# Kernel optimization log

Hardware: AMD Instinct MI355X
Metric: run time of the kernel (lower is better)

The kernel has to match this reference:

```python
import jax, jax.numpy as jnp
import numpy as np

# Module config (matches init_kwargs); num_heads must be 1 for the original
# torch code to type-check (score_proj: Linear(d_model, num_heads) applied to
# a head_dim-sized last axis, then squeeze(-1)).
B, S, D, H = 4, 512, 256, 1
DH = D // H  # head_dim == d_model when H == 1


def _linear_init(k, out_f, in_f):
    bound = 1.0 / np.sqrt(in_f)
    kw, kb = jax.random.split(k)
    W = jax.random.uniform(kw, (out_f, in_f), jnp.float32, -bound, bound)
    b = jax.random.uniform(kb, (out_f,), jnp.float32, -bound, bound)
    return W, b


def setup_inputs() -> dict:
    key = jax.random.key(0)
    ks = jax.random.split(key, 8)
    Wq, bq = _linear_init(ks[3], D, D)
    Wk, bk = _linear_init(ks[4], D, D)
    Wv, bv = _linear_init(ks[5], D, D)
    Ws, bs = _linear_init(ks[6], H, D)   # score_proj: d_model -> num_heads
    Wo, bo = _linear_init(ks[7], D, D)
    return {
        "query": jax.random.normal(ks[0], (B, S, D), jnp.float32),
        "key": jax.random.normal(ks[1], (B, S, D), jnp.float32),
        "value": jax.random.normal(ks[2], (B, S, D), jnp.float32),
        "Wq": Wq, "bq": bq, "Wk": Wk, "bk": bk, "Wv": Wv, "bv": bv,
        "Ws": Ws, "bs": bs, "Wo": Wo, "bo": bo,
    }


def reference(query, key, value, Wq, bq, Wk, bk, Wv, bv, Ws, bs, Wo, bo):
    b, s, _ = query.shape
    # Projections, split into heads: (B, H, S, DH)
    q = (query @ Wq.T + bq).reshape(b, s, H, DH).transpose(0, 2, 1, 3)
    k = (key @ Wk.T + bk).reshape(b, s, H, DH).transpose(0, 2, 1, 3)
    v = (value @ Wv.T + bv).reshape(b, s, H, DH).transpose(0, 2, 1, 3)
    # Bahdanau additive scores: tanh of pairwise sum -> (B, H, Sq, Sk, DH)
    t = jnp.tanh(q[:, :, :, None, :] + k[:, :, None, :, :])
    # score_proj (out_features == 1 when H == 1), then squeeze(-1)
    scores = jnp.einsum('bhqkd,od->bhqko', t, Ws) + bs  # (B,H,Sq,Sk,1)
    scores = scores[..., 0]                              # (B,H,Sq,Sk)
    attn = jax.nn.softmax(scores, axis=-1)
    # Weighted sum of values, merge heads back: (B, S, D)
    attended = jnp.einsum('bhqk,bhkd->bqhd', attn, v).reshape(b, s, D)
    out = attended @ Wo.T + bo  # dropout p=0.0 (eval) -> identity
    return out, attn
```

## Files before the change

### kernel.cpp

```cpp
#include <hip/hip_runtime.h>

typedef __attribute__((ext_vector_type(8))) short short8;
typedef __attribute__((ext_vector_type(4))) float f32x4;

constexpr int BATCH = 4;
constexpr int SEQ   = 512;
constexpr int DM    = 256;

#define MFMA(a,b,c) __builtin_amdgcn_mfma_f32_16x16x32_bf16((a),(b),(c),0,0,0)

__device__ __forceinline__ unsigned short bf16h(float x) {
    unsigned u = __float_as_uint(x);
    return (unsigned short)((u + 0x7FFF + ((u >> 16) & 1)) >> 16);
}
__device__ __forceinline__ float bf16f(unsigned short h) {
    return __uint_as_float(((unsigned)h) << 16);
}
__device__ __forceinline__ float exp2x_clamped(float x) {
    x = fminf(5.0f, fmaxf(-5.0f, x));
    return __builtin_amdgcn_exp2f(x * 2.8853900817779268f);
}
__device__ __forceinline__ void cvt8(const float* s, int4& h, int4& l) {
    unsigned hw[8], lw[8];
    #pragma unroll
    for (int j = 0; j < 8; ++j) {
        unsigned short hb = bf16h(s[j]);
        hw[j] = hb;
        lw[j] = bf16h(s[j] - bf16f(hb));
    }
    h.x = (int)(hw[0] | (hw[1] << 16)); h.y = (int)(hw[2] | (hw[3] << 16));
    h.z = (int)(hw[4] | (hw[5] << 16)); h.w = (int)(hw[6] | (hw[7] << 16));
    l.x = (int)(lw[0] | (lw[1] << 16)); l.y = (int)(lw[2] | (lw[3] << 16));
    l.z = (int)(lw[4] | (lw[5] << 16)); l.w = (int)(lw[6] | (lw[7] << 16));
}

template<int EPI, int ASRC, int BSRC>
__device__ __forceinline__ void mfma_core(
    const ushort* __restrict__ Ah, const ushort* __restrict__ Al,
    const float*  __restrict__ A0, const float*  __restrict__ A1, long ldA,
    const ushort* __restrict__ Bh, const ushort* __restrict__ Bl,
    const float*  __restrict__ B0, long ldB,
    float* __restrict__ C, long ldC, const float* __restrict__ bias,
    ushort* __restrict__ Th, ushort* __restrict__ Tl, long ldT)
{
    __shared__ short lds[32768];
    const int tid = threadIdx.x;
    const int i0 = tid, i1 = tid + 256;
    const int r0 = ((i0 >> 7) << 4) | (i0 & 15), r1 = ((i1 >> 7) << 4) | (i1 & 15);
    const int c0 = ((i0 >> 4) & 7) * 8,          c1 = ((i1 >> 4) & 7) * 8;
    const long a0o = (long)r0 * ldA + c0, a1o = (long)r1 * ldA + c1;
    const long b0o = (long)r0 * ldB + c0, b1o = (long)r1 * ldB + c1;

    int4 rah0, rah1, ral0, ral1, rbh0, rbh1, rbl0, rbl1;
    float4 fa00, fa01, fa10, fa11, ga00, ga01, ga10, ga11;
    float4 gb00, gb01, gb10, gb11;

    auto issue_loads = [&](int it) {
        long off = (long)it * 64;
        if constexpr (ASRC != 0) {
            fa00 = *(const float4*)(A0 + a0o + off); fa01 = *(const float4*)(A0 + a0o + off + 4);
            fa10 = *(const float4*)(A0 + a1o + off); fa11 = *(const float4*)(A0 + a1o + off + 4);
            if constexpr (ASRC == 2) {
                ga00 = *(const float4*)(A1 + a0o + off); ga01 = *(const float4*)(A1 + a0o + off + 4);
                ga10 = *(const float4*)(A1 + a1o + off); ga11 = *(const float4*)(A1 + a1o + off + 4);
            }
        } else {
            rah0 = *(const int4*)(Ah + a0o + off); rah1 = *(const int4*)(Ah + a1o + off);
            ral0 = *(const int4*)(Al + a0o + off); ral1 = *(const int4*)(Al + a1o + off);
        }
        if constexpr (BSRC == 1) {
            gb00 = *(const float4*)(B0 + b0o + off); gb01 = *(const float4*)(B0 + b0o + off + 4);
            gb10 = *(const float4*)(B0 + b1o + off); gb11 = *(const float4*)(B0 + b1o + off + 4);
        } else {
            rbh0 = *(const int4*)(Bh + b0o + off); rbh1 = *(const int4*)(Bh + b1o + off);
            rbl0 = *(const int4*)(Bl + b0o + off); rbl1 = *(const int4*)(Bl + b1o + off);
        }
    };
    auto write_lds = [&](int buf) {
        const int bo = buf * 16384;
        if constexpr (ASRC != 0) {
            float s0[8], s1[8];
            if constexpr (ASRC == 2) {
                s0[0]=fa00.x+ga00.x; s0[1]=fa00.y+ga00.y; s0[2]=fa00.z+ga00.z; s0[3]=fa00.w+ga00.w;
                s0[4]=fa01.x+ga01.x; s0[5]=fa01.y+ga01.y; s0[6]=fa01.z+ga01.z; s0[7]=fa01.w+ga01.w;
                s1[0]=fa10.x+ga10.x; s1[1]=fa10.y+ga10.y; s1[2]=fa10.z+ga10.z; s1[3]=fa10.w+ga10.w;
                s1[4]=fa11.x+ga11.x; s1[5]=fa11.y+ga11.y; s1[6]=fa11.z+ga11.z; s1[7]=fa11.w+ga11.w;
            } else {
                s0[0]=fa00.x; s0[1]=fa00.y; s0[2]=fa00.z; s0[3]=fa00.w;
                s0[4]=fa01.x; s0[5]=fa01.y; s0[6]=fa01.z; s0[7]=fa01.w;
                s1[0]=fa10.x; s1[1]=fa10.y; s1[2]=fa10.z; s1[3]=fa10.w;
                s1[4]=fa11.x; s1[5]=fa11.y; s1[6]=fa11.z; s1[7]=fa11.w;
            }
            int4 h, l2;
            cvt8(s0, h, l2);
            *(int4*)&lds[bo + i0 * 8] = h; *(int4*)&lds[bo + 4096 + i0 * 8] = l2;
            cvt8(s1, h, l2);
            *(int4*)&lds[bo + i1 * 8] = h; *(int4*)&lds[bo + 4096 + i1 * 8] = l2;
        } else {
            *(int4*)&lds[bo + i0 * 8] = rah0;        *(int4*)&lds[bo + i1 * 8] = rah1;
            *(int4*)&lds[bo + 4096 + i0 * 8] = ral0; *(int4*)&lds[bo + 4096 + i1 * 8] = ral1;
        }
        if constexpr (BSRC == 1) {
            float s0[8] = {gb00.x, gb00.y, gb00.z, gb00.w, gb01.x, gb01.y, gb01.z, gb01.w};
            float s1[8] = {gb10.x, gb10.y, gb10.z, gb10.w, gb11.x, gb11.y, gb11.z, gb11.w};
            int4 h, l2;
            cvt8(s0, h, l2);
            *(int4*)&lds[bo + 8192 + i0 * 8] = h; *(int4*)&lds[bo + 12288 + i0 * 8] = l2;
            cvt8(s1, h, l2);
            *(int4*)&lds[bo + 8192 + i1 * 8] = h; *(int4*)&lds[bo + 12288 + i1 * 8] = l2;
        } else {
            *(int4*)&lds[bo + 8192  + i0 * 8] = rbh0; *(int4*)&lds[bo + 8192  + i1 * 8] = rbh1;
            *(int4*)&lds[bo + 12288 + i0 * 8] = rbl0; *(int4*)&lds[bo + 12288 + i1 * 8] = rbl1;
        }
    };

    const int l = tid & 63, w = tid >> 6;
    const int ms = (w >> 1) * 2, ns = (w & 1) * 2;
    f32x4 acc00 = {0,0,0,0}, acc01 = {0,0,0,0}, acc10 = {0,0,0,0}, acc11 = {0,0,0,0};

    issue_loads(0);
    write_lds(0);
    __syncthreads();
    for (int it = 0; it < 4; ++it) {
        if (it < 3) issue_loads(it + 1);
        const int bo = (it & 1) * 16384;
        const int lo = l * 8;
        #pragma unroll
        for (int ks = 0; ks < 2; ++ks) {
            short8 a0h = *(const short8*)&lds[bo + ((ms    ) * 2 + ks) * 512 + lo];
            short8 a1h = *(const short8*)&lds[bo + ((ms + 1) * 2 + ks) * 512 + lo];
            short8 a0l = *(const short8*)&lds[bo + 4096 + ((ms    ) * 2 + ks) * 512 + lo];
            short8 a1l = *(const short8*)&lds[bo + 4096 + ((ms + 1) * 2 + ks) * 512 + lo];
            short8 b0h = *(const short8*)&lds[bo + 8192 + ((ns    ) * 2 + ks) * 512 + lo];
            short8 b1h = *(const short8*)&lds[bo + 8192 + ((ns + 1) * 2 + ks) * 512 + lo];
            short8 b0l = *(const short8*)&lds[bo + 12288 + ((ns    ) * 2 + ks) * 512 + lo];
            short8 b1l = *(const short8*)&lds[bo + 12288 + ((ns + 1) * 2 + ks) * 512 + lo];
            acc00 = MFMA(a0h, b0h, acc00); acc00 = MFMA(a0h, b0l, acc00); acc00 = MFMA(a0l, b0h, acc00);
            acc01 = MFMA(a0h, b1h, acc01); acc01 = MFMA(a0h, b1l, acc01); acc01 = MFMA(a0l, b1h, acc01);
            acc10 = MFMA(a1h, b0h, acc10); acc10 = MFMA(a1h, b0l, acc10); acc10 = MFMA(a1l, b0h, acc10);
            acc11 = MFMA(a1h, b1h, acc11); acc11 = MFMA(a1h, b1l, acc11); acc11 = MFMA(a1l, b1h, acc11);
        }
        if (it < 3) {
            write_lds((it + 1) & 1);
            __syncthreads();
        }
    }

    auto epi = [&](int i, int j, f32x4 a) {
        const int n  = (ns + j) * 16 + (l & 15);
        const int mb = (ms + i) * 16 + (l >> 4) * 4;
        if constexpr (EPI == 1) {
            float bb = bias[n];
            float x0 = a.x + bb, x1 = a.y + bb, x2 = a.z + bb, x3 = a.w + bb;
            unsigned short h0 = bf16h(x0), h1 = bf16h(x1), h2 = bf16h(x2), h3 = bf16h(x3);
            int2 ph, pl;
            ph.x = (int)(h0 | ((unsigned)h1 << 16));
            ph.y = (int)(h2 | ((unsigned)h3 << 16));
            pl.x = (int)(bf16h(x0 - bf16f(h0)) | ((unsigned)bf16h(x1 - bf16f(h1)) << 16));
            pl.y = (int)(bf16h(x2 - bf16f(h2)) | ((unsigned)bf16h(x3 - bf16f(h3)) << 16));
            *(int2*)&Th[(long)n * ldT + mb] = ph;
            *(int2*)&Tl[(long)n * ldT + mb] = pl;
        } else {
            float bb = (EPI == 2) ? 0.f : bias[n];
            float xs[4] = {a.x, a.y, a.z, a.w};
            #pragma unroll
            for (int r = 0; r < 4; ++r) {
                float x = xs[r] + bb;
                if constexpr (EPI == 0) x = exp2x_clamped(x);
                C[(long)(mb + r) * ldC + n] = x;
            }
        }
    };
    epi(0, 0, acc00); epi(0, 1, acc01); epi(1, 0, acc10); epi(1, 1, acc11);
}

__global__ __launch_bounds__(256) void proj_mfma(
    const float* __restrict__ q, const float* __restrict__ k, const float* __restrict__ v,
    const float* __restrict__ Wq, const float* __restrict__ Wk, const float* __restrict__ Wv,
    const float* bq, const float* bk, const float* bv,
    float* Eq, float* Ek, ushort* vpTh, ushort* vpTl)
{
    const int z = blockIdx.z;
    const long m0 = blockIdx.x * 64, n0 = blockIdx.y * 64;
    const float* A; const float* B; const float* bias;
    if (z == 0)      { A = q; B = Wq; bias = bq; }
    else if (z == 1) { A = k; B = Wk; bias = bk; }
    else             { A = v; B = Wv; bias = bv; }
    A += m0 * 256; B += n0 * 256; bias += n0;
    if (z < 2) {
        float* C = (z ? Ek : Eq) + m0 * 256 + n0;
        mfma_core<0, 1, 1>(nullptr, nullptr, A, nullptr, 256,
                           nullptr, nullptr, B, 256,
                           C, 256, bias, nullptr, nullptr, 0);
    } else {
        mfma_core<1, 1, 1>(nullptr, nullptr, A, nullptr, 256,
                           nullptr, nullptr, B, 256,
                           nullptr, 0, bias,
                           vpTh + n0 * 2048 + m0, vpTl + n0 * 2048 + m0, 2048);
    }
}

__global__ __launch_bounds__(256) void attnv_mfma(
    const ushort* attn_h, const ushort* attn_l,
    const ushort* vpTh, const ushort* vpTl, float* att0, float* att1)
{
    const int z = blockIdx.z, b = z >> 1, h = z & 1;
    const long m0 = blockIdx.x * 64, n0 = blockIdx.y * 64;
    const long arow = (long)b * SEQ + m0;
    const ushort* Ah = attn_h + arow * SEQ + h * 256;
    const ushort* Al = attn_l + arow * SEQ + h * 256;
    const ushort* Bh = vpTh + n0 * 2048 + (long)b * SEQ + h * 256;
    const ushort* Bl = vpTl + n0 * 2048 + (long)b * SEQ + h * 256;
    float* C = (h ? att1 : att0) + arow * DM + n0;
    mfma_core<2, 0, 0>(Ah, Al, nullptr, nullptr, SEQ,
                       Bh, Bl, nullptr, 2048,
                       C, DM, nullptr, nullptr, nullptr, 0);
}

__global__ __launch_bounds__(256) void out_mfma(
    const float* att0, const float* att1,
    const float* Wo, const float* bo, float* out)
{
    const long m0 = blockIdx.x * 64, n0 = blockIdx.y * 64;
    mfma_core<3, 2, 1>(nullptr, nullptr, att0 + m0 * 256, att1 + m0 * 256, 256,
                       nullptr, nullptr, Wo + n0 * 256, 256,
                       out + m0 * 256 + n0, 256, bo + n0, nullptr, nullptr, 0);
}

__global__ __launch_bounds__(256) void scores_kernel(
    const float* __restrict__ Eq, const float* __restrict__ Ek,
    const float* __restrict__ Ws, float* __restrict__ part)
{
    __shared__ __align__(16) float qL[64][68];
    __shared__ __align__(16) float kL[64][68];
    const int z = blockIdx.z;
    const int b = z >> 1, c = z & 1;
    const int q0 = blockIdx.x * 64, k0 = blockIdx.y * 64;
    const int tid = threadIdx.x;
    const int qi = tid >> 4, ki = tid & 15;

    float acc[4][4] = {};
    for (int cc = 0; cc < 2; ++cc) {
        const int c0 = c * 128 + cc * 64;
        const float* Eqb = Eq + ((long)b * SEQ + q0) * DM + c0;
        const float* Ekb = Ek + ((long)b * SEQ + k0) * DM + c0;
        if (cc) __syncthreads();
        #pragma unroll
        for (int i = 0; i < 4; ++i) {
            int f = i * 256 + tid;
            int r = f >> 4, col = (f & 15) << 2;
            *(float4*)&qL[r][col] = *(const float4*)(Eqb + (long)r * DM + col);
            *(float4*)&kL[r][col] = *(const float4*)(Ekb + (long)r * DM + col);
        }
        __syncthreads();
        #pragma unroll 2
        for (int d = 0; d < 64; d += 4) {
            float4 w4 = *(const float4*)(Ws + c0 + d);
            float4 av[4], bv[4];
            #pragma unroll
            for (int i = 0; i < 4; ++i) av[i] = *(const float4*)&qL[qi + 16 * i][d];
            #pragma unroll
            for (int j = 0; j < 4; ++j) bv[j] = *(const float4*)&kL[ki + 16 * j][d];
            #pragma unroll
            for (int i = 0; i < 4; ++i)
                #pragma unroll
                for (int j = 0; j < 4; ++j) {
                    float xp = fmaf(av[i].x, bv[j].x, 1.0f);
                    float yp = fmaf(av[i].y, bv[j].y, 1.0f);
                    float zp = fmaf(av[i].z, bv[j].z, 1.0f);
                    float wp = fmaf(av[i].w, bv[j].w, 1.0f);
                    float xy = xp * yp, zw = zp * wp;
                    float n1 = fmaf(w4.x, yp, w4.y * xp);
                    float n2 = fmaf(w4.z, wp, w4.w * zp);
                    float num = fmaf(n1, zw, n2 * xy);
                    acc[i][j] = fmaf(num, __builtin_amdgcn_rcpf(xy * zw), acc[i][j]);
                }
        }
    }

    float* pb = part + (long)c * (BATCH * SEQ * SEQ) + (long)b * SEQ * SEQ;
    #pragma unroll
    for (int i = 0; i < 4; ++i) {
        float* row = pb + (long)(q0 + qi + 16 * i) * SEQ + k0 + ki;
        #pragma unroll
        for (int j = 0; j < 4; ++j) row[16 * j] = acc[i][j];
    }
}

__global__ __launch_bounds__(256) void softmax_kernel(
    const float* __restrict__ part, float* __restrict__ attn,
    ushort* __restrict__ attn_h, ushort* __restrict__ attn_l)
{
    __shared__ float red[8];
    const int tid = threadIdx.x;
    const long row = blockIdx.x;
    constexpr long PS = (long)BATCH * SEQ * SEQ;
    const float* p = part + row * SEQ + tid * 2;
    float2 v0 = *(const float2*)(p);
    float2 v1 = *(const float2*)(p + PS);
    float sx = -2.0f * (v0.x + v1.x);
    float sy = -2.0f * (v0.y + v1.y);

    float m = fmaxf(sx, sy);
    #pragma unroll
    for (int off = 32; off; off >>= 1) m = fmaxf(m, __shfl_xor(m, off));
    int wave = tid >> 6;
    if ((tid & 63) == 0) red[wave] = m;
    __syncthreads();
    m = fmaxf(fmaxf(red[0], red[1]), fmaxf(red[2], red[3]));
    constexpr float L2E = 1.4426950408889634f;
    float e0 = __builtin_amdgcn_exp2f((sx - m) * L2E);
    float e1 = __builtin_amdgcn_exp2f((sy - m) * L2E);
    float s = e0 + e1;
    #pragma unroll
    for (int off = 32; off; off >>= 1) s += __shfl_xor(s, off);
    if ((tid & 63) == 0) red[4 + wave] = s;
    __syncthreads();
    float tot = (red[4] + red[5]) + (red[6] + red[7]);
    float inv = __builtin_amdgcn_rcpf(tot);
    float2 o; o.x = e0 * inv; o.y = e1 * inv;
    *(float2*)(attn + row * SEQ + tid * 2) = o;

    unsigned short h0 = bf16h(o.x), h1 = bf16h(o.y);
    unsigned hp = h0 | ((unsigned)h1 << 16);
    unsigned lp = bf16h(o.x - bf16f(h0)) | ((unsigned)bf16h(o.y - bf16f(h1)) << 16);
    *(unsigned*)&attn_h[row * SEQ + tid * 2] = hp;
    *(unsigned*)&attn_l[row * SEQ + tid * 2] = lp;
}

extern "C" void kernel_launch(void* const* d_in, const int* in_sizes, int n_in,
                              void* d_out, int out_size, void* d_ws, size_t ws_size,
                              hipStream_t stream) {
    const float* query = (const float*)d_in[0];
    const float* key   = (const float*)d_in[1];
    const float* value = (const float*)d_in[2];
    const float* Wq = (const float*)d_in[3];
    const float* bq = (const float*)d_in[4];
    const float* Wk = (const float*)d_in[5];
    const float* bk = (const float*)d_in[6];
    const float* Wv = (const float*)d_in[7];
    const float* bv = (const float*)d_in[8];
    const float* Ws = (const float*)d_in[9];
    const float* Wo = (const float*)d_in[11];
    const float* bo = (const float*)d_in[12];

    float* out  = (float*)d_out;
    float* attn = (float*)d_out + (long)BATCH * SEQ * DM;

    float* ws = (float*)d_ws;
    float* Eq   = ws;
    float* Ek   = ws + 524288;
    float* part = ws + 1048576;
    float* att0 = part;
    float* att1 = part + 524288;
    ushort* u = (ushort*)(ws + 1048576 + 2097152);
    ushort* vpTh   = u;              ushort* vpTl   = vpTh + 524288;
    ushort* attn_h = vpTl + 524288;  ushort* attn_l = attn_h + 1048576;

    proj_mfma    <<<dim3(32, 4, 3), 256, 0, stream>>>(query, key, value,
                                                      Wq, Wk, Wv, bq, bk, bv,
                                                      Eq, Ek, vpTh, vpTl);
    scores_kernel<<<dim3(8, 8, 8),  256, 0, stream>>>(Eq, Ek, Ws, part);
    softmax_kernel<<<dim3(2048),    256, 0, stream>>>(part, attn, attn_h, attn_l);
    attnv_mfma   <<<dim3(8, 4, 8),  256, 0, stream>>>(attn_h, attn_l, vpTh, vpTl, att0, att1);
    out_mfma     <<<dim3(32, 4),    256, 0, stream>>>(att0, att1, Wo, bo, out);
}
```

Before: 74.93 us.

## Fold output projection into value projection and merge attn-V with output GEMM

Precomputes Wvo = Wo·Wv and bvo = Wo·bv in a small kernel, projects values straight through the combined weight, and computes out = attn·(V·Wvoᵀ) + bo in a single GEMM with full-K accumulation. This removes the separate output GEMM and the two-way K-split partial buffers. The shared GEMM core changes from double-buffered LDS to a single buffer with a variable K loop, trading prefetch overlap for less LDS use. Softmax drops its max-subtraction pass because tanh keeps scores bounded, which removes one block reduction and barrier.

```diff
diff --git a/kernel.cpp b/kernel.cpp
--- a/kernel.cpp
+++ b/kernel.cpp
@@ -34,16 +34,39 @@
     l.z = (int)(lw[4] | (lw[5] << 16)); l.w = (int)(lw[6] | (lw[7] << 16));
 }
 
+__global__ __launch_bounds__(256) void wvo_kernel(
+    const float* __restrict__ Wo, const float* __restrict__ Wv,
+    const float* __restrict__ bv, float* __restrict__ Wvo,
+    float* __restrict__ bvo)
+{
+    __shared__ float red[4];
+    const int j = blockIdx.x, t = threadIdx.x;
+    const float* wrow = Wo + (long)j * 256;
+    float acc = 0.f;
+    #pragma unroll 4
+    for (int d = 0; d < 256; ++d)
+        acc = fmaf(wrow[d], Wv[(long)d * 256 + t], acc);
+    Wvo[(long)j * 256 + t] = acc;
+
+    float pb = wrow[t] * bv[t];
+    #pragma unroll
+    for (int off = 32; off; off >>= 1) pb += __shfl_xor(pb, off);
+    if ((t & 63) == 0) red[t >> 6] = pb;
+    __syncthreads();
+    if (t == 0) bvo[j] = (red[0] + red[1]) + (red[2] + red[3]);
+}
+
 template<int EPI, int ASRC, int BSRC>
 __device__ __forceinline__ void mfma_core(
     const ushort* __restrict__ Ah, const ushort* __restrict__ Al,
-    const float*  __restrict__ A0, const float*  __restrict__ A1, long ldA,
+    const float*  __restrict__ A0, long ldA,
     const ushort* __restrict__ Bh, const ushort* __restrict__ Bl,
     const float*  __restrict__ B0, long ldB,
+    int K,
     float* __restrict__ C, long ldC, const float* __restrict__ bias,
     ushort* __restrict__ Th, ushort* __restrict__ Tl, long ldT)
 {
-    __shared__ short lds[32768];
+    __shared__ short lds[16384];
     const int tid = threadIdx.x;
     const int i0 = tid, i1 = tid + 256;
     const int r0 = ((i0 >> 7) << 4) | (i0 & 15), r1 = ((i1 >> 7) << 4) | (i1 & 15);
@@ -52,18 +75,13 @@
     const long b0o = (long)r0 * ldB + c0, b1o = (long)r1 * ldB + c1;
 
     int4 rah0, rah1, ral0, ral1, rbh0, rbh1, rbl0, rbl1;
-    float4 fa00, fa01, fa10, fa11, ga00, ga01, ga10, ga11;
-    float4 gb00, gb01, gb10, gb11;
+    float4 fa00, fa01, fa10, fa11, gb00, gb01, gb10, gb11;
 
     auto issue_loads = [&](int it) {
         long off = (long)it * 64;
-        if constexpr (ASRC != 0) {
+        if constexpr (ASRC == 1) {
             fa00 = *(const float4*)(A0 + a0o + off); fa01 = *(const float4*)(A0 + a0o + off + 4);
             fa10 = *(const float4*)(A0 + a1o + off); fa11 = *(const float4*)(A0 + a1o + off + 4);
-            if constexpr (ASRC == 2) {
-                ga00 = *(const float4*)(A1 + a0o + off); ga01 = *(const float4*)(A1 + a0o + off + 4);
-                ga10 = *(const float4*)(A1 + a1o + off); ga11 = *(const float4*)(A1 + a1o + off + 4);
-            }
         } else {
             rah0 = *(const int4*)(Ah + a0o + off); rah1 = *(const int4*)(Ah + a1o + off);
             ral0 = *(const int4*)(Al + a0o + off); ral1 = *(const int4*)(Al + a1o + off);
@@ -76,41 +94,30 @@
             rbl0 = *(const int4*)(Bl + b0o + off); rbl1 = *(const int4*)(Bl + b1o + off);
         }
     };
-    auto write_lds = [&](int buf) {
-        const int bo = buf * 16384;
-        if constexpr (ASRC != 0) {
-            float s0[8], s1[8];
-            if constexpr (ASRC == 2) {
-                s0[0]=fa00.x+ga00.x; s0[1]=fa00.y+ga00.y; s0[2]=fa00.z+ga00.z; s0[3]=fa00.w+ga00.w;
-                s0[4]=fa01.x+ga01.x; s0[5]=fa01.y+ga01.y; s0[6]=fa01.z+ga01.z; s0[7]=fa01.w+ga01.w;
-                s1[0]=fa10.x+ga10.x; s1[1]=fa10.y+ga10.y; s1[2]=fa10.z+ga10.z; s1[3]=fa10.w+ga10.w;
-                s1[4]=fa11.x+ga11.x; s1[5]=fa11.y+ga11.y; s1[6]=fa11.z+ga11.z; s1[7]=fa11.w+ga11.w;
-            } else {
-                s0[0]=fa00.x; s0[1]=fa00.y; s0[2]=fa00.z; s0[3]=fa00.w;
-                s0[4]=fa01.x; s0[5]=fa01.y; s0[6]=fa01.z; s0[7]=fa01.w;
-                s1[0]=fa10.x; s1[1]=fa10.y; s1[2]=fa10.z; s1[3]=fa10.w;
-                s1[4]=fa11.x; s1[5]=fa11.y; s1[6]=fa11.z; s1[7]=fa11.w;
-            }
+    auto write_lds = [&]() {
+        if constexpr (ASRC == 1) {
+            float s0[8] = {fa00.x, fa00.y, fa00.z, fa00.w, fa01.x, fa01.y, fa01.z, fa01.w};
+            float s1[8] = {fa10.x, fa10.y, fa10.z, fa10.w, fa11.x, fa11.y, fa11.z, fa11.w};
             int4 h, l2;
             cvt8(s0, h, l2);
-            *(int4*)&lds[bo + i0 * 8] = h; *(int4*)&lds[bo + 4096 + i0 * 8] = l2;
+            *(int4*)&lds[i0 * 8] = h; *(int4*)&lds[4096 + i0 * 8] = l2;
             cvt8(s1, h, l2);
-            *(int4*)&lds[bo + i1 * 8] = h; *(int4*)&lds[bo + 4096 + i1 * 8] = l2;
-        } else {
-            *(int4*)&lds[bo + i0 * 8] = rah0;        *(int4*)&lds[bo + i1 * 8] = rah1;
-            *(int4*)&lds[bo + 4096 + i0 * 8] = ral0; *(int4*)&lds[bo + 4096 + i1 * 8] = ral1;
+            *(int4*)&lds[i1 * 8] = h; *(int4*)&lds[4096 + i1 * 8] = l2;
+        } else {
+            *(int4*)&lds[i0 * 8] = rah0;        *(int4*)&lds[i1 * 8] = rah1;
+            *(int4*)&lds[4096 + i0 * 8] = ral0; *(int4*)&lds[4096 + i1 * 8] = ral1;
         }
         if constexpr (BSRC == 1) {
             float s0[8] = {gb00.x, gb00.y, gb00.z, gb00.w, gb01.x, gb01.y, gb01.z, gb01.w};
             float s1[8] = {gb10.x, gb10.y, gb10.z, gb10.w, gb11.x, gb11.y, gb11.z, gb11.w};
             int4 h, l2;
             cvt8(s0, h, l2);
-            *(int4*)&lds[bo + 8192 + i0 * 8] = h; *(int4*)&lds[bo + 12288 + i0 * 8] = l2;
+            *(int4*)&lds[8192 + i0 * 8] = h; *(int4*)&lds[12288 + i0 * 8] = l2;
             cvt8(s1, h, l2);
-            *(int4*)&lds[bo + 8192 + i1 * 8] = h; *(int4*)&lds[bo + 12288 + i1 * 8] = l2;
-        } else {
-            *(int4*)&lds[bo + 8192  + i0 * 8] = rbh0; *(int4*)&lds[bo + 8192  + i1 * 8] = rbh1;
-            *(int4*)&lds[bo + 12288 + i0 * 8] = rbl0; *(int4*)&lds[bo + 12288 + i1 * 8] = rbl1;
+            *(int4*)&lds[8192 + i1 * 8] = h; *(int4*)&lds[12288 + i1 * 8] = l2;
+        } else {
+            *(int4*)&lds[8192  + i0 * 8] = rbh0; *(int4*)&lds[8192  + i1 * 8] = rbh1;
+            *(int4*)&lds[12288 + i0 * 8] = rbl0; *(int4*)&lds[12288 + i1 * 8] = rbl1;
         }
     };
 
@@ -118,32 +125,29 @@
     const int ms = (w >> 1) * 2, ns = (w & 1) * 2;
     f32x4 acc00 = {0,0,0,0}, acc01 = {0,0,0,0}, acc10 = {0,0,0,0}, acc11 = {0,0,0,0};
 
+    const int iters = K >> 6;
     issue_loads(0);
-    write_lds(0);
-    __syncthreads();
-    for (int it = 0; it < 4; ++it) {
-        if (it < 3) issue_loads(it + 1);
-        const int bo = (it & 1) * 16384;
+    for (int it = 0; it < iters; ++it) {
+        write_lds();
+        __syncthreads();
+        if (it + 1 < iters) issue_loads(it + 1);
         const int lo = l * 8;
         #pragma unroll
         for (int ks = 0; ks < 2; ++ks) {
-            short8 a0h = *(const short8*)&lds[bo + ((ms    ) * 2 + ks) * 512 + lo];
-            short8 a1h = *(const short8*)&lds[bo + ((ms + 1) * 2 + ks) * 512 + lo];
-            short8 a0l = *(const short8*)&lds[bo + 4096 + ((ms    ) * 2 + ks) * 512 + lo];
-            short8 a1l = *(const short8*)&lds[bo + 4096 + ((ms + 1) * 2 + ks) * 512 + lo];
-            short8 b0h = *(const short8*)&lds[bo + 8192 + ((ns    ) * 2 + ks) * 512 + lo];
-            short8 b1h = *(const short8*)&lds[bo + 8192 + ((ns + 1) * 2 + ks) * 512 + lo];
-            short8 b0l = *(const short8*)&lds[bo + 12288 + ((ns    ) * 2 + ks) * 512 + lo];
-            short8 b1l = *(const short8*)&lds[bo + 12288 + ((ns + 1) * 2 + ks) * 512 + lo];
+            short8 a0h = *(const short8*)&lds[((ms    ) * 2 + ks) * 512 + lo];
+            short8 a1h = *(const short8*)&lds[((ms + 1) * 2 + ks) * 512 + lo];
+            short8 a0l = *(const short8*)&lds[4096 + ((ms    ) * 2 + ks) * 512 + lo];
+            short8 a1l = *(const short8*)&lds[4096 + ((ms + 1) * 2 + ks) * 512 + lo];
+            short8 b0h = *(const short8*)&lds[8192 + ((ns    ) * 2 + ks) * 512 + lo];
+            short8 b1h = *(const short8*)&lds[8192 + ((ns + 1) * 2 + ks) * 512 + lo];
+            short8 b0l = *(const short8*)&lds[12288 + ((ns    ) * 2 + ks) * 512 + lo];
+            short8 b1l = *(const short8*)&lds[12288 + ((ns + 1) * 2 + ks) * 512 + lo];
             acc00 = MFMA(a0h, b0h, acc00); acc00 = MFMA(a0h, b0l, acc00); acc00 = MFMA(a0l, b0h, acc00);
             acc01 = MFMA(a0h, b1h, acc01); acc01 = MFMA(a0h, b1l, acc01); acc01 = MFMA(a0l, b1h, acc01);
             acc10 = MFMA(a1h, b0h, acc10); acc10 = MFMA(a1h, b0l, acc10); acc10 = MFMA(a1l, b0h, acc10);
             acc11 = MFMA(a1h, b1h, acc11); acc11 = MFMA(a1h, b1l, acc11); acc11 = MFMA(a1l, b1h, acc11);
         }
-        if (it < 3) {
-            write_lds((it + 1) & 1);
-            __syncthreads();
-        }
+        __syncthreads();
     }
 
     auto epi = [&](int i, int j, f32x4 a) {
@@ -161,7 +165,7 @@
             *(int2*)&Th[(long)n * ldT + mb] = ph;
             *(int2*)&Tl[(long)n * ldT + mb] = pl;
         } else {
-            float bb = (EPI == 2) ? 0.f : bias[n];
+            float bb = bias[n];
             float xs[4] = {a.x, a.y, a.z, a.w};
             #pragma unroll
             for (int r = 0; r < 4; ++r) {
@@ -176,55 +180,43 @@
 
 __global__ __launch_bounds__(256) void proj_mfma(
     const float* __restrict__ q, const float* __restrict__ k, const float* __restrict__ v,
-    const float* __restrict__ Wq, const float* __restrict__ Wk, const float* __restrict__ Wv,
-    const float* bq, const float* bk, const float* bv,
-    float* Eq, float* Ek, ushort* vpTh, ushort* vpTl)
+    const float* __restrict__ Wq, const float* __restrict__ Wk, const float* __restrict__ Wvo,
+    const float* bq, const float* bk, const float* bvo,
+    float* Eq, float* Ek, ushort* pvoTh, ushort* pvoTl)
 {
     const int z = blockIdx.z;
     const long m0 = blockIdx.x * 64, n0 = blockIdx.y * 64;
     const float* A; const float* B; const float* bias;
-    if (z == 0)      { A = q; B = Wq; bias = bq; }
-    else if (z == 1) { A = k; B = Wk; bias = bk; }
-    else             { A = v; B = Wv; bias = bv; }
+    if (z == 0)      { A = q; B = Wq;  bias = bq; }
+    else if (z == 1) { A = k; B = Wk;  bias = bk; }
+    else             { A = v; B = Wvo; bias = bvo; }
     A += m0 * 256; B += n0 * 256; bias += n0;
     if (z < 2) {
         float* C = (z ? Ek : Eq) + m0 * 256 + n0;
-        mfma_core<0, 1, 1>(nullptr, nullptr, A, nullptr, 256,
-                           nullptr, nullptr, B, 256,
+        mfma_core<0, 1, 1>(nullptr, nullptr, A, 256,
+                           nullptr, nullptr, B, 256, 256,
                            C, 256, bias, nullptr, nullptr, 0);
     } else {
-        mfma_core<1, 1, 1>(nullptr, nullptr, A, nullptr, 256,
-                           nullptr, nullptr, B, 256,
+        mfma_core<1, 1, 1>(nullptr, nullptr, A, 256,
+                           nullptr, nullptr, B, 256, 256,
                            nullptr, 0, bias,
-                           vpTh + n0 * 2048 + m0, vpTl + n0 * 2048 + m0, 2048);
-    }
-}
-
-__global__ __launch_bounds__(256) void attnv_mfma(
-    const ushort* attn_h, const ushort* attn_l,
-    const ushort* vpTh, const ushort* vpTl, float* att0, float* att1)
-{
-    const int z = blockIdx.z, b = z >> 1, h = z & 1;
+                           pvoTh + n0 * 2048 + m0, pvoTl + n0 * 2048 + m0, 2048);
+    }
+}
+
+__global__ __launch_bounds__(256) void final_mfma(
+    const ushort* ah, const ushort* al,
+    const ushort* pvoTh, const ushort* pvoTl,
+    const float* bo, float* out)
+{
+    const int b = blockIdx.z;
     const long m0 = blockIdx.x * 64, n0 = blockIdx.y * 64;
     const long arow = (long)b * SEQ + m0;
-    const ushort* Ah = attn_h + arow * SEQ + h * 256;
-    const ushort* Al = attn_l + arow * SEQ + h * 256;
-    const ushort* Bh = vpTh + n0 * 2048 + (long)b * SEQ + h * 256;
-    const ushort* Bl = vpTl + n0 * 2048 + (long)b * SEQ + h * 256;
-    float* C = (h ? att1 : att0) + arow * DM + n0;
-    mfma_core<2, 0, 0>(Ah, Al, nullptr, nullptr, SEQ,
-                       Bh, Bl, nullptr, 2048,
-                       C, DM, nullptr, nullptr, nullptr, 0);
-}
-
-__global__ __launch_bounds__(256) void out_mfma(
-    const float* att0, const float* att1,
-    const float* Wo, const float* bo, float* out)
-{
-    const long m0 = blockIdx.x * 64, n0 = blockIdx.y * 64;
-    mfma_core<3, 2, 1>(nullptr, nullptr, att0 + m0 * 256, att1 + m0 * 256, 256,
-                       nullptr, nullptr, Wo + n0 * 256, 256,
-                       out + m0 * 256 + n0, 256, bo + n0, nullptr, nullptr, 0);
+    mfma_core<2, 0, 0>(ah + arow * 512, al + arow * 512, nullptr, 512,
+                       pvoTh + n0 * 2048 + (long)b * 512,
+                       pvoTl + n0 * 2048 + (long)b * 512, nullptr, 2048, 512,
+                       out + arow * 256 + n0, 256, bo + n0,
+                       nullptr, nullptr, 0);
 }
 
 __global__ __launch_bounds__(256) void scores_kernel(
@@ -291,32 +283,23 @@
     const float* __restrict__ part, float* __restrict__ attn,
     ushort* __restrict__ attn_h, ushort* __restrict__ attn_l)
 {
-    __shared__ float red[8];
+    __shared__ float red[4];
     const int tid = threadIdx.x;
     const long row = blockIdx.x;
     constexpr long PS = (long)BATCH * SEQ * SEQ;
     const float* p = part + row * SEQ + tid * 2;
     float2 v0 = *(const float2*)(p);
     float2 v1 = *(const float2*)(p + PS);
-    float sx = -2.0f * (v0.x + v1.x);
-    float sy = -2.0f * (v0.y + v1.y);
-
-    float m = fmaxf(sx, sy);
-    #pragma unroll
-    for (int off = 32; off; off >>= 1) m = fmaxf(m, __shfl_xor(m, off));
-    int wave = tid >> 6;
-    if ((tid & 63) == 0) red[wave] = m;
-    __syncthreads();
-    m = fmaxf(fmaxf(red[0], red[1]), fmaxf(red[2], red[3]));
-    constexpr float L2E = 1.4426950408889634f;
-    float e0 = __builtin_amdgcn_exp2f((sx - m) * L2E);
-    float e1 = __builtin_amdgcn_exp2f((sy - m) * L2E);
+    constexpr float NL2E = -2.0f * 1.4426950408889634f;
+    float e0 = __builtin_amdgcn_exp2f(NL2E * (v0.x + v1.x));
+    float e1 = __builtin_amdgcn_exp2f(NL2E * (v0.y + v1.y));
     float s = e0 + e1;
     #pragma unroll
     for (int off = 32; off; off >>= 1) s += __shfl_xor(s, off);
-    if ((tid & 63) == 0) red[4 + wave] = s;
+    int wave = tid >> 6;
+    if ((tid & 63) == 0) red[wave] = s;
     __syncthreads();
-    float tot = (red[4] + red[5]) + (red[6] + red[7]);
+    float tot = (red[0] + red[1]) + (red[2] + red[3]);
     float inv = __builtin_amdgcn_rcpf(tot);
     float2 o; o.x = e0 * inv; o.y = e1 * inv;
     *(float2*)(attn + row * SEQ + tid * 2) = o;
@@ -351,17 +334,17 @@
     float* Eq   = ws;
     float* Ek   = ws + 524288;
     float* part = ws + 1048576;
-    float* att0 = part;
-    float* att1 = part + 524288;
-    ushort* u = (ushort*)(ws + 1048576 + 2097152);
-    ushort* vpTh   = u;              ushort* vpTl   = vpTh + 524288;
-    ushort* attn_h = vpTl + 524288;  ushort* attn_l = attn_h + 1048576;
-
+    float* Wvo  = ws + 1048576 + 2097152;
+    float* bvo  = Wvo + 65536;
+    ushort* u = (ushort*)(bvo + 256);
+    ushort* pvoTh = u;                 ushort* pvoTl = pvoTh + 524288;
+    ushort* ah    = pvoTl + 524288;    ushort* al    = ah + 1048576;
+
+    wvo_kernel   <<<dim3(256),      256, 0, stream>>>(Wo, Wv, bv, Wvo, bvo);
     proj_mfma    <<<dim3(32, 4, 3), 256, 0, stream>>>(query, key, value,
-                                                      Wq, Wk, Wv, bq, bk, bv,
-                                                      Eq, Ek, vpTh, vpTl);
+                                                      Wq, Wk, Wvo, bq, bk, bvo,
+                                                      Eq, Ek, pvoTh, pvoTl);
     scores_kernel<<<dim3(8, 8, 8),  256, 0, stream>>>(Eq, Ek, Ws, part);
-    softmax_kernel<<<dim3(2048),    256, 0, stream>>>(part, attn, attn_h, attn_l);
-    attnv_mfma   <<<dim3(8, 4, 8),  256, 0, stream>>>(attn_h, attn_l, vpTh, vpTl, att0, att1);
-    out_mfma     <<<dim3(32, 4),    256, 0, stream>>>(att0, att1, Wo, bo, out);
-}
+    softmax_kernel<<<dim3(2048),    256, 0, stream>>>(part, attn, ah, al);
+    final_mfma   <<<dim3(8, 4, 4),  256, 0, stream>>>(ah, al, pvoTh, pvoTl, bo, out);
+}
```

Result: slower. 80.92 us (+8.0%).
